# Kernel optimization log

Hardware: AMD Instinct MI355X
Metric: run time of the kernel (lower is better)

Reference implementation:

```python
import jax, jax.numpy as jnp
import numpy as np

B, S, D = 4, 2048, 1024
H = 16
DH = D // H
MLP_DIM = 4096
EPS = 1e-6


def setup_inputs() -> dict:
    key = jax.random.key(0)
    ks = jax.random.split(key, 16)
    sd = lambda fi, fo: (1.0 / np.sqrt(fi))
    return {
        "x": jax.random.normal(ks[0], (B, S, D), jnp.float32),
        "Wq": jax.random.normal(ks[1], (D, D), jnp.float32) * sd(D, D),
        "bq": jnp.zeros((D,), jnp.float32),
        "Wk": jax.random.normal(ks[2], (D, D), jnp.float32) * sd(D, D),
        "bk": jnp.zeros((D,), jnp.float32),
        "Wv": jax.random.normal(ks[3], (D, D), jnp.float32) * sd(D, D),
        "bv": jnp.zeros((D,), jnp.float32),
        "Wo": jax.random.normal(ks[4], (D, D), jnp.float32) * sd(D, D),
        "bo": jnp.zeros((D,), jnp.float32),
        "ln1_g": jnp.ones((D,), jnp.float32),
        "ln1_b": jnp.zeros((D,), jnp.float32),
        "ln2_g": jnp.ones((D,), jnp.float32),
        "ln2_b": jnp.zeros((D,), jnp.float32),
        "W1": jax.random.normal(ks[5], (D, MLP_DIM), jnp.float32) * sd(D, MLP_DIM),
        "b1": jax.random.normal(ks[6], (MLP_DIM,), jnp.float32) * 1e-6,
        "W2": jax.random.normal(ks[7], (MLP_DIM, D), jnp.float32) * sd(MLP_DIM, D),
        "b2": jax.random.normal(ks[8], (D,), jnp.float32) * 1e-6,
    }


def _layernorm(x, g, b):
    mu = jnp.mean(x, axis=-1, keepdims=True)
    var = jnp.mean(jnp.square(x - mu), axis=-1, keepdims=True)
    return (x - mu) * jax.lax.rsqrt(var + EPS) * g + b


def reference(x, Wq, bq, Wk, bk, Wv, bv, Wo, bo,
              ln1_g, ln1_b, ln2_g, ln2_b, W1, b1, W2, b2):
    h = x
    xn = _layernorm(x, ln1_g, ln1_b)
    # Q/K/V: [B,S,D] -> [B,H,S,DH]
    def split_heads(t):
        return t.reshape(B, S, H, DH).transpose(0, 2, 1, 3)
    Q = split_heads(xn @ Wq + bq)
    K = split_heads(xn @ Wk + bk)
    V = split_heads(xn @ Wv + bv)
    scores = jnp.einsum("bhqd,bhkd->bhqk", Q, K) / np.sqrt(DH).astype(np.float32)
    a = jax.nn.softmax(scores, axis=-1)
    r = jnp.einsum("bhqk,bhkd->bhqd", a, V)          # [B,H,S,DH]
    r = r.transpose(0, 2, 1, 3).reshape(B, S, D)      # merge heads
    r = r @ Wo + bo
    x = r + h
    h = x
    xn = _layernorm(x, ln2_g, ln2_b)
    m = jax.nn.gelu(xn @ W1 + b1, approximate=False)
    m = m @ W2 + b2
    return m + h
```

## Files before the change

### kernel.cpp

```cpp
#include <hip/hip_runtime.h>
#include <math.h>

#define B_ 4
#define S_ 2048
#define D_ 1024
#define H_ 16
#define MLP_ 4096
#define MROWS 8192

typedef __attribute__((ext_vector_type(4))) float f32x4;
typedef __attribute__((ext_vector_type(16))) float f32x16;
typedef __attribute__((ext_vector_type(8))) __bf16 bf16x8;
typedef __attribute__((ext_vector_type(4))) __bf16 bf16x4;
typedef __attribute__((ext_vector_type(8))) unsigned short us8;
typedef unsigned short u16;
typedef unsigned int u32;

__device__ __forceinline__ void gload16(const void* g, void* l) {
    __builtin_amdgcn_global_load_lds((const __attribute__((address_space(1))) u32*)g,
                                     (__attribute__((address_space(3))) u32*)l, 16, 0, 0);
}

__device__ __forceinline__ float gelu_f(float v) {
    float p = fmaf(v * v, 0.044715f, 1.0f);
    float e = __builtin_amdgcn_exp2f(v * 2.3022089f * p);
    float r = __builtin_amdgcn_rcpf(e + 1.0f);
    return v - v * r;
}

__global__ __launch_bounds__(256) void ln_bf16_k(const float* __restrict__ x,
                                                 const float* __restrict__ g,
                                                 const float* __restrict__ b,
                                                 u16* __restrict__ y) {
    int row = blockIdx.x;
    int tid = threadIdx.x;
    const float* xr = x + (size_t)row * D_;
    f32x4 v = *(const f32x4*)(xr + tid * 4);
    float s = v.x + v.y + v.z + v.w;
    float ss = v.x * v.x + v.y * v.y + v.z * v.z + v.w * v.w;
    for (int off = 32; off > 0; off >>= 1) {
        s += __shfl_down(s, off, 64);
        ss += __shfl_down(ss, off, 64);
    }
    __shared__ float rs[4], rss[4];
    int lane = tid & 63, wid = tid >> 6;
    if (lane == 0) { rs[wid] = s; rss[wid] = ss; }
    __syncthreads();
    s = rs[0] + rs[1] + rs[2] + rs[3];
    ss = rss[0] + rss[1] + rss[2] + rss[3];
    float mu = s * (1.0f / D_);
    float var = ss * (1.0f / D_) - mu * mu;
    float inv = rsqrtf(var + 1e-6f);
    f32x4 gg = *(const f32x4*)(g + tid * 4);
    f32x4 bb = *(const f32x4*)(b + tid * 4);
    bf16x4 o = {(__bf16)((v.x - mu) * inv * gg.x + bb.x),
                (__bf16)((v.y - mu) * inv * gg.y + bb.y),
                (__bf16)((v.z - mu) * inv * gg.z + bb.z),
                (__bf16)((v.w - mu) * inv * gg.w + bb.w)};
    *(bf16x4*)(y + (size_t)row * D_ + tid * 4) = o;
}

__global__ void pack3_k(const float* __restrict__ a, const float* __restrict__ b,
                        const float* __restrict__ c, float* __restrict__ o, float s0) {
    const float* s = blockIdx.x == 0 ? a : (blockIdx.x == 1 ? b : c);
    float sc = blockIdx.x == 0 ? s0 : 1.0f;
    o[blockIdx.x * 1024 + threadIdx.x] = s[threadIdx.x] * sc;
}

__global__ __launch_bounds__(256) void wtrans_k(const float* __restrict__ W,
                                                u16* __restrict__ Wt, int K, int N,
                                                float scale) {
    __shared__ float T[32][33];
    int tid = threadIdx.x;
    int k0 = blockIdx.y * 32, n0 = blockIdx.x * 32;
    int r = tid >> 3, c4 = (tid & 7) * 4;
    f32x4 v = *(const f32x4*)&W[(size_t)(k0 + r) * N + n0 + c4];
    T[r][c4 + 0] = v.x; T[r][c4 + 1] = v.y; T[r][c4 + 2] = v.z; T[r][c4 + 3] = v.w;
    __syncthreads();
    int n = tid >> 3, kk = (tid & 7) * 4;
    bf16x4 o = {(__bf16)(T[kk + 0][n] * scale), (__bf16)(T[kk + 1][n] * scale),
                (__bf16)(T[kk + 2][n] * scale), (__bf16)(T[kk + 3][n] * scale)};
    *(bf16x4*)&Wt[(size_t)(n0 + n) * K + k0 + kk] = o;
}

__device__ __forceinline__ int sigma_perm(int s) {
    return (s & 48) | (s & 3) | (((s >> 2) & 1) << 3) | (((s >> 3) & 1) << 2);
}
__global__ __launch_bounds__(256) void vtrans_k(const u16* __restrict__ QKV,
                                                u16* __restrict__ Vt) {
    __shared__ u16 T[64][80];
    int tid = threadIdx.x;
    int s0 = blockIdx.x * 64;
    int bh = blockIdx.y, b = bh >> 4, h = bh & 15;
    int r = tid >> 2, c0 = (tid & 3) * 16;
    const u16* src = QKV + (size_t)(b * S_ + s0 + r) * 3072 + 2048 + h * 64 + c0;
    us8 v0 = *(const us8*)src;
    us8 v1 = *(const us8*)(src + 8);
    *(us8*)&T[r][c0] = v0;
    *(us8*)&T[r][c0 + 8] = v1;
    __syncthreads();
    int dh = tid >> 2, s8 = (tid & 3) * 16;
    us8 o0, o1;
#pragma unroll
    for (int i = 0; i < 8; ++i) {
        o0[i] = T[sigma_perm(s8 + i)][dh];
        o1[i] = T[sigma_perm(s8 + 8 + i)][dh];
    }
    u16* dst = Vt + (size_t)(bh * 64 + dh) * S_ + s0 + s8;
    *(us8*)dst = o0;
    *(us8*)(dst + 8) = o1;
}

template <int EPI>
__global__ __launch_bounds__(256) void gemm_bf16(const u16* __restrict__ A,
                                                 const u16* __restrict__ Wt,
                                                 const float* __restrict__ bias,
                                                 const float* __restrict__ res,
                                                 void* __restrict__ Cout,
                                                 int M, int N, int K) {
    __shared__ u16 As[3][128 * 32];
    __shared__ u16 Bs[3][128 * 32];
    const int tid = threadIdx.x;
    const int lane = tid & 63;
    const int w = tid >> 6;
    const int nwg = gridDim.x * gridDim.y;
    int hw = blockIdx.x + gridDim.x * blockIdx.y;
    int lg = (hw & 7) * (nwg >> 3) + (hw >> 3);
    const int row0 = (lg / gridDim.x) * 128;
    const int col0 = (lg % gridDim.x) * 128;
    const int l15 = lane & 15, l16 = lane >> 4;
    const int wr = w >> 1, wc = w & 1;

    f32x4 acc[4][4];
#pragma unroll
    for (int i = 0; i < 4; ++i)
#pragma unroll
        for (int j = 0; j < 4; ++j) acc[i][j] = (f32x4){0.f, 0.f, 0.f, 0.f};

    const int srow = w * 32 + (lane >> 2);
    const size_t sboff = (size_t)(((lane & 3) ^ ((lane >> 3) & 3)) * 16);
    const char* Ag = (const char*)A + ((size_t)(row0 + srow) * K) * 2 + sboff;
    const char* Bg = (const char*)Wt + ((size_t)(col0 + srow) * K) * 2 + sboff;
    const size_t rstep = (size_t)16 * K * 2;
    const int woff = w * 2048;
    const int T = K >> 5;

#define STAGE(t, bi) do {                                      \
        size_t kb = (size_t)(t) << 6;                          \
        char* asw = (char*)As + (bi) * 8192 + woff;            \
        char* bsw = (char*)Bs + (bi) * 8192 + woff;            \
        gload16(Ag + kb, asw);                                 \
        gload16(Ag + kb + rstep, asw + 1024);                  \
        gload16(Bg + kb, bsw);                                 \
        gload16(Bg + kb + rstep, bsw + 1024);                  \
    } while (0)

    STAGE(0, 0);
    STAGE(1, 1);
    asm volatile("s_waitcnt vmcnt(4)" ::: "memory");
    __builtin_amdgcn_s_barrier();
    __builtin_amdgcn_sched_barrier(0);

    const int ksw = (l16 ^ ((l15 >> 1) & 3)) << 4;
    int bi = 0;
    for (int t = 0; t < T; ++t) {
        if (t + 2 < T) {
            int nb = bi + 2; if (nb >= 3) nb -= 3;
            STAGE(t + 2, nb);
        }
        const char* Ab = (const char*)As + bi * 8192;
        const char* Bb = (const char*)Bs + bi * 8192;
        bf16x8 af[4], bfr[4];
#pragma unroll
        for (int f = 0; f < 4; ++f) {
            af[f] = *(const bf16x8*)(Ab + (size_t)(wr * 64 + f * 16 + l15) * 64 + ksw);
            bfr[f] = *(const bf16x8*)(Bb + (size_t)(wc * 64 + f * 16 + l15) * 64 + ksw);
        }
        __builtin_amdgcn_s_setprio(1);
#pragma unroll
        for (int fi = 0; fi < 4; ++fi)
#pragma unroll
            for (int fj = 0; fj < 4; ++fj)
                acc[fi][fj] = __builtin_amdgcn_mfma_f32_16x16x32_bf16(af[fi], bfr[fj], acc[fi][fj], 0, 0, 0);
        __builtin_amdgcn_s_setprio(0);
        if (t + 2 < T) {
            asm volatile("s_waitcnt vmcnt(4)" ::: "memory");
        } else {
            asm volatile("s_waitcnt vmcnt(0)" ::: "memory");
        }
        __builtin_amdgcn_s_barrier();
        __builtin_amdgcn_sched_barrier(0);
        if (++bi >= 3) bi = 0;
    }
#undef STAGE

    const int rb = row0 + wr * 64 + (l16 << 2);
    const int cb = col0 + wc * 64 + l15;
#pragma unroll
    for (int fi = 0; fi < 4; ++fi)
#pragma unroll
        for (int fj = 0; fj < 4; ++fj) {
            int c = cb + fj * 16;
            float bv = bias[c];
#pragma unroll
            for (int rr = 0; rr < 4; ++rr) {
                int r = rb + fi * 16 + rr;
                float v = acc[fi][fj][rr] + bv;
                if (EPI == 1) v = gelu_f(v);
                if (EPI == 2) {
                    v += res[(size_t)r * N + c];
                    ((float*)Cout)[(size_t)r * N + c] = v;
                } else {
                    ((__bf16*)Cout)[(size_t)r * N + c] = (__bf16)v;
                }
            }
        }
}

__global__ __launch_bounds__(256) void attn_mfma(const u16* __restrict__ QKV,
                                                 const u16* __restrict__ Vt,
                                                 u16* __restrict__ O) {
    __shared__ u16 Ks[2][64 * 64];
    __shared__ u16 Vs[2][64 * 64];
    const int tid = threadIdx.x, lane = tid & 63, w = tid >> 6;
    int hw = blockIdx.x + gridDim.x * blockIdx.y;
    int lg = (hw & 7) * 128 + (hw >> 3);
    const int bh = lg >> 4, b = bh >> 4, h = bh & 15;
    const int q0 = (lg & 15) * 128;
    const int l31 = lane & 31, lh = lane >> 5;

    const u16* Qp = QKV + (size_t)(b * S_ + q0 + w * 32 + l31) * 3072 + h * 64 + lh * 8;
    bf16x8 qf[4];
    qf[0] = *(const bf16x8*)(Qp);
    qf[1] = *(const bf16x8*)(Qp + 16);
    qf[2] = *(const bf16x8*)(Qp + 32);
    qf[3] = *(const bf16x8*)(Qp + 48);

    f32x16 oacc[2];
    f32x16 lacc;
#pragma unroll
    for (int i = 0; i < 16; ++i) { oacc[0][i] = 0.f; oacc[1][i] = 0.f; lacc[i] = 0.f; }
    bf16x8 ones;
#pragma unroll
    for (int j = 0; j < 8; ++j) ones[j] = (__bf16)1.0f;

    const int sr = lane >> 3;
    const size_t soff = (size_t)(((lane & 7) ^ sr) << 4);
    const char* Kg = (const char*)QKV + ((size_t)b * S_ * 3072 + 1024 + h * 64) * 2;
    const char* Vg = (const char*)Vt + (size_t)bh * 64 * S_ * 2;

    const char* kp0 = Kg + (size_t)(w * 16 + sr) * 6144 + soff;
    const char* kp1 = kp0 + 8 * 6144;
    const char* vp0 = Vg + (size_t)(w * 16 + sr) * 4096 + soff;
    const char* vp1 = vp0 + 8 * 4096;
    const size_t KADV = 64 * 6144;
    const size_t VADV = 128;
    char* ksA = (char*)Ks[0] + w * 2048;
    char* ksB = (char*)Ks[1] + w * 2048;
    char* vsA = (char*)Vs[0] + w * 2048;
    char* vsB = (char*)Vs[1] + w * 2048;

    gload16(kp0, ksA); gload16(kp1, ksA + 1024);
    gload16(vp0, vsA); gload16(vp1, vsA + 1024);
    kp0 += KADV; kp1 += KADV; vp0 += VADV; vp1 += VADV;
    __syncthreads();

    for (int kt = 0; kt < S_ / 64; ++kt) {
        const int cur = kt & 1;
        if (kt < S_ / 64 - 1) {
            char* kd = cur ? ksA : ksB;
            char* vd = cur ? vsA : vsB;
            gload16(kp0, kd); gload16(kp1, kd + 1024);
            gload16(vp0, vd); gload16(vp1, vd + 1024);
            kp0 += KADV; kp1 += KADV; vp0 += VADV; vp1 += VADV;
        }

        const char* Kb_ = (const char*)Ks[cur];
        f32x16 sfr[2];
        __builtin_amdgcn_s_setprio(1);
#pragma unroll
        for (int kh = 0; kh < 2; ++kh) {
            int r = kh * 32 + l31;
            int rsw = (r & 7) << 4;
            const char* Kr = Kb_ + r * 128;
            f32x16 t;
#pragma unroll
            for (int i = 0; i < 16; ++i) t[i] = 0.f;
#pragma unroll
            for (int ds = 0; ds < 4; ++ds) {
                bf16x8 kf = *(const bf16x8*)(Kr + ((((ds * 2 + lh) << 4)) ^ rsw));
                t = __builtin_amdgcn_mfma_f32_32x32x16_bf16(kf, qf[ds], t, 0, 0, 0);
            }
            sfr[kh] = t;
        }
        __builtin_amdgcn_s_setprio(0);

        float pv0[16], pv1[16];
#pragma unroll
        for (int i = 0; i < 16; ++i) {
            pv0[i] = __builtin_amdgcn_exp2f(sfr[0][i]);
            pv1[i] = __builtin_amdgcn_exp2f(sfr[1][i]);
        }

        bf16x8 pf[4];
#pragma unroll
        for (int j = 0; j < 8; ++j) {
            pf[0][j] = (__bf16)pv0[j];
            pf[1][j] = (__bf16)pv0[8 + j];
            pf[2][j] = (__bf16)pv1[j];
            pf[3][j] = (__bf16)pv1[8 + j];
        }

        {
            const char* Vb_ = (const char*)Vs[cur];
            __builtin_amdgcn_s_setprio(1);
#pragma unroll
            for (int ks = 0; ks < 4; ++ks)
                lacc = __builtin_amdgcn_mfma_f32_32x32x16_bf16(ones, pf[ks], lacc, 0, 0, 0);
#pragma unroll
            for (int dh = 0; dh < 2; ++dh) {
                int r = dh * 32 + l31;
                int rsw = (r & 7) << 4;
                const char* Vr = Vb_ + r * 128;
#pragma unroll
                for (int ks = 0; ks < 4; ++ks) {
                    bf16x8 vf = *(const bf16x8*)(Vr + ((((ks * 2 + lh) << 4)) ^ rsw));
                    oacc[dh] = __builtin_amdgcn_mfma_f32_32x32x16_bf16(vf, pf[ks], oacc[dh], 0, 0, 0);
                }
            }
            __builtin_amdgcn_s_setprio(0);
        }
        __syncthreads();
    }

    float invl = 1.0f / lacc[0];
    char* Og = (char*)O + ((size_t)(b * S_ + q0 + w * 32 + l31) * 1024 + h * 64) * 2;
#pragma unroll
    for (int dh = 0; dh < 2; ++dh)
#pragma unroll
        for (int t4 = 0; t4 < 4; ++t4) {
            int db = dh * 32 + t4 * 8 + lh * 4;
            bf16x4 ov = {(__bf16)(oacc[dh][t4 * 4] * invl),
                         (__bf16)(oacc[dh][t4 * 4 + 1] * invl),
                         (__bf16)(oacc[dh][t4 * 4 + 2] * invl),
                         (__bf16)(oacc[dh][t4 * 4 + 3] * invl)};
            *(bf16x4*)(Og + db * 2) = ov;
        }
}

extern "C" void kernel_launch(void* const* d_in, const int* in_sizes, int n_in,
                              void* d_out, int out_size, void* d_ws, size_t ws_size,
                              hipStream_t stream) {
    const float* x     = (const float*)d_in[0];
    const float* Wq    = (const float*)d_in[1];
    const float* bq    = (const float*)d_in[2];
    const float* Wk    = (const float*)d_in[3];
    const float* bk    = (const float*)d_in[4];
    const float* Wv    = (const float*)d_in[5];
    const float* bv    = (const float*)d_in[6];
    const float* Wo    = (const float*)d_in[7];
    const float* bo    = (const float*)d_in[8];
    const float* ln1_g = (const float*)d_in[9];
    const float* ln1_b = (const float*)d_in[10];
    const float* ln2_g = (const float*)d_in[11];
    const float* ln2_b = (const float*)d_in[12];
    const float* W1    = (const float*)d_in[13];
    const float* b1    = (const float*)d_in[14];
    const float* W2    = (const float*)d_in[15];
    const float* b2    = (const float*)d_in[16];
    float* out = (float*)d_out;
    const float C2 = 0.18033688011112f;

    const size_t MB = 1ull << 20;
    char* ws = (char*)d_ws;
    u16* QKVb = (u16*)(ws + 0 * MB);
    u16* aout = (u16*)(ws + 48 * MB);
    u16* mid  = (u16*)(ws + 0 * MB);
    float* x2 = (float*)(ws + 64 * MB);
    float* bqkv = (float*)(ws + 64 * MB);
    u16* xn   = (u16*)(ws + 96 * MB);
    u16* Vt   = (u16*)(ws + 96 * MB);
    u16* xn2  = (u16*)(ws + 96 * MB);
    u16* Wqkvt = (u16*)(ws + 112 * MB);
    u16* Wot  = Wqkvt + (size_t)3072 * D_;
    u16* W1t  = (u16*)(ws + 112 * MB);
    u16* W2t  = (u16*)(ws + 120 * MB);

    wtrans_k<<<dim3(32, 32), 256, 0, stream>>>(Wq, Wqkvt, D_, D_, C2);
    wtrans_k<<<dim3(32, 32), 256, 0, stream>>>(Wk, Wqkvt + (size_t)D_ * D_, D_, D_, 1.0f);
    wtrans_k<<<dim3(32, 32), 256, 0, stream>>>(Wv, Wqkvt + (size_t)2 * D_ * D_, D_, D_, 1.0f);
    wtrans_k<<<dim3(32, 32), 256, 0, stream>>>(Wo, Wot, D_, D_, 1.0f);
    wtrans_k<<<dim3(32, 128), 256, 0, stream>>>(W2, W2t, MLP_, D_, 1.0f);
    pack3_k<<<3, 1024, 0, stream>>>(bq, bk, bv, bqkv, C2);

    ln_bf16_k<<<MROWS, 256, 0, stream>>>(x, ln1_g, ln1_b, xn);
    gemm_bf16<0><<<dim3(24, 64), 256, 0, stream>>>(xn, Wqkvt, bqkv, nullptr, QKVb, MROWS, 3072, D_);
    vtrans_k<<<dim3(32, 64), 256, 0, stream>>>(QKVb, Vt);
    attn_mfma<<<dim3(16, 64), 256, 0, stream>>>(QKVb, Vt, aout);
    gemm_bf16<2><<<dim3(8, 64), 256, 0, stream>>>(aout, Wot, bo, x, x2, MROWS, D_, D_);
    wtrans_k<<<dim3(128, 32), 256, 0, stream>>>(W1, W1t, D_, MLP_, 1.0f);
    ln_bf16_k<<<MROWS, 256, 0, stream>>>(x2, ln2_g, ln2_b, xn2);
    gemm_bf16<1><<<dim3(32, 64), 256, 0, stream>>>(xn2, W1t, b1, nullptr, mid, MROWS, MLP_, D_);
    gemm_bf16<2><<<dim3(8, 64), 256, 0, stream>>>(mid, W2t, b2, x2, (void*)out, MROWS, D_, MLP_);
}
```

Baseline: 425.4 us.

## Add 256x256-tile 8-wave triple-buffered GEMM for QKV and MLP-up projections

Introduces a new bf16 MFMA GEMM kernel with 256x256 output tiles, 512 threads, a three-slot LDS ring fed by direct global-to-LDS loads, and swizzled LDS reads. Prefetch is interleaved with the compute phases and uses priority bumps. It replaces the old 128-tile GEMM for the QKV projection and the GELU MLP-up projection, aiming for more operand reuse and better latency hiding. The cost is higher register and LDS pressure, lower occupancy, and fewer workgroups, which could leave compute units underused.

```diff
diff --git a/kernel.cpp b/kernel.cpp
--- a/kernel.cpp
+++ b/kernel.cpp
@@ -217,6 +217,117 @@
         }
 }
 
+template <int EPI>
+__global__ __launch_bounds__(512) void gemm8p(const u16* __restrict__ A,
+                                              const u16* __restrict__ Wt,
+                                              const float* __restrict__ bias,
+                                              u16* __restrict__ Cout,
+                                              int M, int N, int K) {
+    __shared__ u16 As[3][256 * 32];
+    __shared__ u16 Bs[3][256 * 32];
+    const int tid = threadIdx.x;
+    const int lane = tid & 63;
+    const int w = tid >> 6;
+    const int nwg = gridDim.x * gridDim.y;
+    int hw = blockIdx.x + gridDim.x * blockIdx.y;
+    int lg = (hw & 7) * (nwg >> 3) + (hw >> 3);
+    const int row0 = (lg / gridDim.x) * 256;
+    const int col0 = (lg % gridDim.x) * 256;
+    const int l15 = lane & 15, l16 = lane >> 4;
+    const int wr = w >> 2, wc = w & 3;
+
+    f32x4 acc[8][4];
+#pragma unroll
+    for (int i = 0; i < 8; ++i)
+#pragma unroll
+        for (int j = 0; j < 4; ++j) acc[i][j] = (f32x4){0.f, 0.f, 0.f, 0.f};
+
+    const size_t Kb = (size_t)K * 2;
+    const size_t sboff = (size_t)(((lane & 3) ^ ((lane >> 3) & 3)) * 16);
+    const char* Ag0 = (const char*)A + (size_t)(row0 + w * 16 + (lane >> 2)) * Kb + sboff;
+    const char* Ag1 = Ag0 + 128 * Kb;
+    const char* Bg0 = (const char*)Wt + (size_t)(col0 + w * 16 + (lane >> 2)) * Kb + sboff;
+    const char* Bg1 = Bg0 + 128 * Kb;
+    const int T = K >> 5;
+
+#define STAGE_A8(t, sl) do {                         \
+        size_t kb = (size_t)(t) << 6;                \
+        char* d = (char*)As[sl] + w * 1024;          \
+        gload16(Ag0 + kb, d);                        \
+        gload16(Ag1 + kb, d + 8192);                 \
+    } while (0)
+#define STAGE_B8(t, sl) do {                         \
+        size_t kb = (size_t)(t) << 6;                \
+        char* d = (char*)Bs[sl] + w * 1024;          \
+        gload16(Bg0 + kb, d);                        \
+        gload16(Bg1 + kb, d + 8192);                 \
+    } while (0)
+
+    STAGE_A8(0, 0); STAGE_B8(0, 0);
+    STAGE_A8(1, 1); STAGE_B8(1, 1);
+    asm volatile("s_waitcnt vmcnt(4)" ::: "memory");
+    __builtin_amdgcn_s_barrier();
+    __builtin_amdgcn_sched_barrier(0);
+
+    const int ksw = (l16 ^ ((l15 >> 1) & 3)) << 4;
+    int slot = 0;
+    for (int t = 0; t < T; ++t) {
+        const char* Ab = (const char*)As[slot];
+        const char* Bb = (const char*)Bs[slot];
+        int s2 = slot + 2; if (s2 >= 3) s2 -= 3;
+#pragma unroll
+        for (int p = 0; p < 2; ++p) {
+            bf16x8 af[4], bfv[4];
+#pragma unroll
+            for (int m = 0; m < 4; ++m)
+                af[m] = *(const bf16x8*)(Ab + (size_t)(wr * 128 + p * 64 + m * 16 + l15) * 64 + ksw);
+#pragma unroll
+            for (int n = 0; n < 4; ++n)
+                bfv[n] = *(const bf16x8*)(Bb + (size_t)(wc * 64 + n * 16 + l15) * 64 + ksw);
+            if (t + 2 < T) {
+                if (p == 0) STAGE_A8(t + 2, s2);
+                else        STAGE_B8(t + 2, s2);
+            }
+            __builtin_amdgcn_s_barrier();
+            asm volatile("s_waitcnt lgkmcnt(0)" ::: "memory");
+            __builtin_amdgcn_sched_barrier(0);
+            __builtin_amdgcn_s_setprio(1);
+#pragma unroll
+            for (int m = 0; m < 4; ++m)
+#pragma unroll
+                for (int n = 0; n < 4; ++n)
+                    acc[p * 4 + m][n] = __builtin_amdgcn_mfma_f32_16x16x32_bf16(af[m], bfv[n], acc[p * 4 + m][n], 0, 0, 0);
+            __builtin_amdgcn_s_setprio(0);
+            if (p == 1) {
+                if (t + 2 < T) asm volatile("s_waitcnt vmcnt(4)" ::: "memory");
+                else           asm volatile("s_waitcnt vmcnt(0)" ::: "memory");
+            }
+            __builtin_amdgcn_s_barrier();
+            __builtin_amdgcn_sched_barrier(0);
+        }
+        if (++slot >= 3) slot = 0;
+    }
+#undef STAGE_A8
+#undef STAGE_B8
+
+    const int cbase = col0 + wc * 64 + l15;
+#pragma unroll
+    for (int mi = 0; mi < 8; ++mi) {
+        int rb = row0 + wr * 128 + (mi >> 2) * 64 + (mi & 3) * 16 + (l16 << 2);
+#pragma unroll
+        for (int n = 0; n < 4; ++n) {
+            int c = cbase + n * 16;
+            float bv = bias[c];
+#pragma unroll
+            for (int rr = 0; rr < 4; ++rr) {
+                float v = acc[mi][n][rr] + bv;
+                if (EPI == 1) v = gelu_f(v);
+                ((__bf16*)Cout)[(size_t)(rb + rr) * N + c] = (__bf16)v;
+            }
+        }
+    }
+}
+
 __global__ __launch_bounds__(256) void attn_mfma(const u16* __restrict__ QKV,
                                                  const u16* __restrict__ Vt,
                                                  u16* __restrict__ O) {
@@ -394,12 +505,12 @@
     pack3_k<<<3, 1024, 0, stream>>>(bq, bk, bv, bqkv, C2);
 
     ln_bf16_k<<<MROWS, 256, 0, stream>>>(x, ln1_g, ln1_b, xn);
-    gemm_bf16<0><<<dim3(24, 64), 256, 0, stream>>>(xn, Wqkvt, bqkv, nullptr, QKVb, MROWS, 3072, D_);
+    gemm8p<0><<<dim3(12, 32), 512, 0, stream>>>(xn, Wqkvt, bqkv, QKVb, MROWS, 3072, D_);
     vtrans_k<<<dim3(32, 64), 256, 0, stream>>>(QKVb, Vt);
     attn_mfma<<<dim3(16, 64), 256, 0, stream>>>(QKVb, Vt, aout);
     gemm_bf16<2><<<dim3(8, 64), 256, 0, stream>>>(aout, Wot, bo, x, x2, MROWS, D_, D_);
     wtrans_k<<<dim3(128, 32), 256, 0, stream>>>(W1, W1t, D_, MLP_, 1.0f);
     ln_bf16_k<<<MROWS, 256, 0, stream>>>(x2, ln2_g, ln2_b, xn2);
-    gemm_bf16<1><<<dim3(32, 64), 256, 0, stream>>>(xn2, W1t, b1, nullptr, mid, MROWS, MLP_, D_);
+    gemm8p<1><<<dim3(16, 32), 512, 0, stream>>>(xn2, W1t, b1, mid, MROWS, MLP_, D_);
     gemm_bf16<2><<<dim3(8, 64), 256, 0, stream>>>(mid, W2t, b2, x2, (void*)out, MROWS, D_, MLP_);
 }
```

After: 425.2 us. No clear change (-0.0%).
